# Performance work log

Measured on AMD Instinct MI355X. Metric: run time of the kernel, lower is better.

Reference implementation:

```python
import jax, jax.numpy as jnp
import numpy as np

R, B, F, C, NCLS = 32, 4096, 256, 4, 1000  # n_rules, batch, n_fea, n_channel, n_cls
K, PAD, POOL = 5, 1, 2                     # kernel_size, padding, pooling_size


def setup_inputs() -> dict:
    key = jax.random.key(0)
    ks = jax.random.split(key, 12)
    L0 = F + 2 * PAD - K + 1          # 254 after conv1
    L1 = L0 // POOL                   # 127 after avgpool1
    L2 = (L1 + 2 * PAD - K + 1) // POOL  # 62 after conv2+avgpool2
    att = C * L2                      # 248 (matches torch att_size formula)
    hid = att // 2                    # 124
    s = lambda k, shape: jax.random.normal(k, shape, dtype=jnp.float32) * 0.05
    return dict(
        data=jax.random.normal(ks[0], (B, F), dtype=jnp.float32),
        proto=s(ks[1], (R, F)),
        conv1_w=s(ks[2], (C, 1, K)), conv1_b=s(ks[3], (C,)),
        conv2_w=s(ks[4], (C, C, K)), conv2_b=s(ks[5], (C,)),
        fc1_w=s(ks[6], (att, hid)), fc1_b=s(ks[7], (hid,)),
        fc2_w=s(ks[8], (hid, 1)), fc2_b=s(ks[9], (1,)),
        consq_w=s(ks[10], (R, F, NCLS)), consq_b=s(ks[11], (R, NCLS)),
        is_train=0,
    )


def _conv1d(x, w, b):
    # x: [N, Cin, L], w: [Cout, Cin, K]
    out = jax.lax.conv_general_dilated(
        x, w, window_strides=(1,), padding=[(PAD, PAD)],
        dimension_numbers=('NCH', 'OIH', 'NCH'))
    return out + b[None, :, None]


def _avgpool2(x):
    # non-overlapping AvgPool1d(2), drops trailing remainder like torch
    L2 = x.shape[-1] // POOL
    return x[..., :L2 * POOL].reshape(x.shape[0], x.shape[1], L2, POOL).mean(-1)


def reference(data, proto, conv1_w, conv1_b, conv2_w, conv2_b,
              fc1_w, fc1_b, fc2_w, fc2_b, consq_w, consq_b, is_train):
    n_batch = data.shape[0]
    # data_diff: [R, B, F] -> shared gating net, fold rules into batch
    diff = (data[None, :, :] - proto[:, None, :]).reshape(R * n_batch, 1, F)
    h = _avgpool2(jax.nn.relu(_conv1d(diff, conv1_w, conv1_b)))
    h = _avgpool2(jax.nn.relu(_conv1d(h, conv2_w, conv2_b)))
    h = h.reshape(R * n_batch, -1)                       # [R*B, att]
    h = jax.nn.relu(h @ fc1_w + fc1_b)                   # [R*B, hid]
    fs_ini = jnp.tanh(h @ fc2_w + fc2_b)                 # [R*B, 1]
    fs_ini = fs_ini.reshape(R, n_batch).T                # cat(dim=1) -> [B, R]
    fs = jax.nn.softmax(fs_ini, axis=1)                  # softmax over rules
    # per-rule experts: grouped matmul [B,F] x [R,F,NCLS]
    expert = jnp.einsum('bf,rfc->rbc', data, consq_w) + consq_b[:, None, :]
    return jnp.einsum('br,rbc->bc', fs, expert)          # [B, NCLS]
```

## Files before the change

### kernel.cpp

```cpp
#include <hip/hip_runtime.h>
#include <hip/hip_bf16.h>

using bf16x8 = __attribute__((ext_vector_type(8))) short;
using f32x4  = __attribute__((ext_vector_type(4))) float;
using v2f    = __attribute__((ext_vector_type(2))) float;

__device__ __forceinline__ unsigned short f2bf_rne(float x) {
    unsigned u = __float_as_uint(x);
    u += 0x7fffu + ((u >> 16) & 1u);
    return (unsigned short)(u >> 16);
}

__device__ __forceinline__ void gload_lds16(const void* g, void* l) {
    __builtin_amdgcn_global_load_lds(
        (const __attribute__((address_space(1))) unsigned int*)g,
        (__attribute__((address_space(3))) unsigned int*)l, 16, 0, 0);
}

constexpr int KP = 8320;
constexpr int KROW = KP * 2;

constexpr size_t OFF_DT  = 0;
constexpr size_t OFF_Q1  = OFF_DT  + (size_t)260 * 4096 * 4;
constexpr size_t OFF_BT  = OFF_Q1  + (size_t)32 * 1024 * 4;
constexpr size_t OFF_C1P = OFF_BT;
constexpr size_t OFF_W1S = OFF_BT  + (size_t)1024 * KP * 2;
constexpr size_t OFF_FSI = OFF_W1S + (size_t)128 * 256 * 2;
constexpr size_t OFF_FS  = OFF_FSI + (size_t)32 * 4096 * 4;
constexpr size_t OFF_ASC = OFF_FS  + (size_t)32 * 4096 * 4;
constexpr size_t OFF_H2  = OFF_ASC;
constexpr size_t OFF_P1  = OFF_ASC + (size_t)4096 * KP * 2;

__global__ __launch_bounds__(256) void k_transpose(const float* __restrict__ data,
                                                   float* __restrict__ dTp) {
    __shared__ float tile[64][65];
    int bx = blockIdx.x & 63;
    int fx = blockIdx.x >> 6;
    int tx = threadIdx.x & 63, ty4 = threadIdx.x >> 6;
#pragma unroll
    for (int i = 0; i < 16; ++i) {
        int ty = ty4 * 16 + i;
        tile[ty][tx] = data[(bx * 64 + ty) * 256 + fx * 64 + tx];
    }
    __syncthreads();
#pragma unroll
    for (int i = 0; i < 16; ++i) {
        int ty = ty4 * 16 + i;
        dTp[(size_t)(fx * 64 + ty + 1) * 4096 + bx * 64 + tx] = tile[tx][ty];
    }
}

__global__ __launch_bounds__(256) void k_zrows(float* __restrict__ dTp) {
    int i = blockIdx.x * 256 + threadIdx.x;
    dTp[i] = 0.f;
    dTp[(size_t)257 * 4096 + i] = 0.f;
}

__global__ __launch_bounds__(256) void k_prep_proto(const float* __restrict__ proto,
                                                    const float* __restrict__ w1,
                                                    const float* __restrict__ b1,
                                                    float* __restrict__ q1p) {
    __shared__ float ps[256];
    __shared__ float w1s[20];
    int r = blockIdx.x, tid = threadIdx.x;
    ps[tid] = proto[r * 256 + tid];
    if (tid < 20) w1s[tid] = w1[tid];
    __syncthreads();
    if (tid < 254) {
#pragma unroll
        for (int c = 0; c < 4; ++c) {
            float s = -b1[c];
#pragma unroll
            for (int k = 0; k < 5; ++k) {
                int x = tid + k - 1;
                float xv = (x >= 0 && x < 256) ? ps[x] : 0.f;
                s += w1s[c * 5 + k] * xv;
            }
            q1p[r * 1024 + c * 256 + tid] = s;
        }
    }
}

__global__ __launch_bounds__(64) void k_prep_c1d(const float* __restrict__ dTp,
                                                 const float* __restrict__ w1,
                                                 float2* __restrict__ c1p) {
    int lane = threadIdx.x;
    int bg = blockIdx.x >> 3, ch = blockIdx.x & 7;
    int l0 = ch << 4;
    int nl = (ch == 7) ? 15 : 16;
    int b = (bg << 6) + lane;
    float w1r[20];
#pragma unroll
    for (int i = 0; i < 20; ++i) w1r[i] = w1[i];
    const float* dp = dTp + (size_t)(2 * l0) * 4096 + b;
    float d[6];
#pragma unroll
    for (int i = 0; i < 6; ++i) d[i] = dp[(size_t)i * 4096];
    dp += (size_t)6 * 4096;
    float2* outp = c1p + b;
    for (int li = 0; li < nl; ++li) {
        int l = l0 + li;
#pragma unroll
        for (int c = 0; c < 4; ++c) {
            float s0 = 0.f, s1 = 0.f;
#pragma unroll
            for (int k = 0; k < 5; ++k) {
                s0 += w1r[c * 5 + k] * d[k];
                s1 += w1r[c * 5 + k] * d[k + 1];
            }
            outp[(size_t)(c * 127 + l) * 4096] = make_float2(s0, s1);
        }
        d[0] = d[2]; d[1] = d[3]; d[2] = d[4]; d[3] = d[5];
        d[4] = dp[0];
        d[5] = dp[4096];
        dp += 8192;
    }
}

__global__ __launch_bounds__(256) void k_castB(const float* __restrict__ cw,
                                               const float* __restrict__ cb,
                                               unsigned short* __restrict__ BT) {
    __shared__ unsigned short L[64 * 137];
    int tid = threadIdx.x;
    int kt = blockIdx.x >> 3, ct = blockIdx.x & 7;
    int k0 = kt << 6, c0 = ct << 7;
#pragma unroll
    for (int i = 0; i < 32; ++i) {
        int flat = i * 256 + tid;
        int cl = flat & 127, kl = flat >> 7;
        int cg = c0 + cl;
        int kg = k0 + kl;
        float v = 0.f;
        if (cg < 1000) {
            if (kg < 8192) v = cw[(size_t)kg * 1000 + cg];
            else if (kg < 8224) v = cb[(size_t)(kg - 8192) * 1000 + cg];
        }
        L[kl * 137 + cl] = f2bf_rne(v);
    }
    __syncthreads();
#pragma unroll
    for (int i = 0; i < 4; ++i) {
        int task = i * 256 + tid;
        int kg = task & 7, cl = task >> 3;
        int base = kg * 8 * 137 + cl;
        unsigned x = (unsigned)L[base] | ((unsigned)L[base + 137] << 16);
        unsigned y = (unsigned)L[base + 2 * 137] | ((unsigned)L[base + 3 * 137] << 16);
        unsigned z = (unsigned)L[base + 4 * 137] | ((unsigned)L[base + 5 * 137] << 16);
        unsigned w = (unsigned)L[base + 6 * 137] | ((unsigned)L[base + 7 * 137] << 16);
        uint4 o; o.x = x; o.y = y; o.z = z; o.w = w;
        int cg = c0 + cl;
        size_t byte = (size_t)cg * KROW + (size_t)(kt << 7) + (size_t)((kg ^ (cg & 7)) << 4);
        *(uint4*)((char*)BT + byte) = o;
    }
}

__global__ __launch_bounds__(256) void k_castW(const float* __restrict__ fc1w,
                                               unsigned short* __restrict__ W1s) {
    int idx = blockIdx.x * 256 + threadIdx.x;
    int col = idx >> 8, k = idx & 255;
    float v = 0.f;
    if (col < 124 && k < 248) {
        int f = (k & 3) * 62 + (k >> 2);
        v = fc1w[f * 124 + col];
    }
    int byte = col * 512 + ((k >> 6) << 7) + ((((k >> 3) & 7) ^ (col & 7)) << 4) + ((k & 7) << 1);
    *(unsigned short*)((char*)W1s + byte) = f2bf_rne(v);
}

__global__ __launch_bounds__(64)
void k_conv2(const float2* __restrict__ c1p,
             const float* __restrict__ q1p,
             const float* __restrict__ w2,
             const float* __restrict__ b2,
             char* __restrict__ h2c) {
    __shared__ unsigned short T[64 * 72];

    int lane = threadIdx.x;
    int job = blockIdx.x;
    int jh = job & 1;
    int bc = (job >> 1) & 63;
    int r  = job >> 7;
    int b0 = bc << 6;
    int rb0 = r * 4096 + b0;
    int j2s = jh ? 32 : 0;

    float w2r[80];
#pragma unroll
    for (int i = 0; i < 80; ++i) w2r[i] = w2[i];
    v2f bb[4];
#pragma unroll
    for (int c = 0; c < 4; ++c) { float t = b2[c]; bb[c][0] = t; bb[c][1] = t; }

    const float* q1row = q1p + r * 1024;
    const float2* cpb = c1p + b0 + lane;

    auto pooled = [&](int c, int l) -> float {
        float2 v = cpb[(size_t)(c * 127 + l) * 4096];
        float2 q = *(const float2*)(q1row + c * 256 + 2 * l);
        return 0.5f * (fmaxf(v.x - q.x, 0.f) + fmaxf(v.y - q.y, 0.f));
    };

    v2f P[4][5];
#pragma unroll
    for (int c = 0; c < 4; ++c) {
        float pv[6];
#pragma unroll
        for (int idx = 0; idx < 6; ++idx) {
            int l = 2 * j2s - 1 + idx;
            pv[idx] = (l < 0) ? 0.f : pooled(c, l);
        }
#pragma unroll
        for (int k = 0; k < 5; ++k) { P[c][k][0] = pv[k]; P[c][k][1] = pv[k + 1]; }
    }

    int j2 = j2s;
#pragma unroll 1
    for (int chunk = 0; chunk < 2; ++chunk) {
        int cnt = (jh && chunk) ? 14 : 16;
#pragma unroll 1
        for (int jj = 0; jj < cnt; ++jj) {
            v2f u[4];
#pragma unroll
            for (int c = 0; c < 4; ++c) u[c] = bb[c];
#pragma unroll
            for (int c = 0; c < 4; ++c)
#pragma unroll
                for (int ci = 0; ci < 4; ++ci)
#pragma unroll
                    for (int k = 0; k < 5; ++k)
                        u[c] += P[ci][k] * w2r[(c * 4 + ci) * 5 + k];
            {
                float h0 = 0.5f * (fmaxf(u[0][0], 0.f) + fmaxf(u[0][1], 0.f));
                float h1 = 0.5f * (fmaxf(u[1][0], 0.f) + fmaxf(u[1][1], 0.f));
                float h2v = 0.5f * (fmaxf(u[2][0], 0.f) + fmaxf(u[2][1], 0.f));
                float h3 = 0.5f * (fmaxf(u[3][0], 0.f) + fmaxf(u[3][1], 0.f));
                uint2 vv;
                vv.x = (unsigned)f2bf_rne(h0) | ((unsigned)f2bf_rne(h1) << 16);
                vv.y = (unsigned)f2bf_rne(h2v) | ((unsigned)f2bf_rne(h3) << 16);
                *(uint2*)(T + lane * 72 + jj * 4) = vv;
            }
            if (!(chunk == 1 && jj == cnt - 1)) {
#pragma unroll
                for (int c = 0; c < 4; ++c) {
                    float n0 = pooled(c, 2 * j2 + 5);
                    float n1 = pooled(c, 2 * j2 + 6);
                    v2f p4v = P[c][4];
                    P[c][0] = P[c][2]; P[c][1] = P[c][3]; P[c][2] = p4v;
                    v2f t3; t3[0] = p4v[1]; t3[1] = n0;
                    v2f t4; t4[0] = n0;     t4[1] = n1;
                    P[c][3] = t3; P[c][4] = t4;
                }
            }
            ++j2;
        }
        if (jh && chunk) {
            uint4 z; z.x = z.y = z.z = z.w = 0u;
            *(uint4*)(T + lane * 72 + 56) = z;
        }
        {
            int chunkIdx = (j2s >> 4) + chunk;
            int g = lane & 7;
#pragma unroll
            for (int i = 0; i < 8; ++i) {
                int sL = i * 8 + (lane >> 3);
                bf16x8 v = *(const bf16x8*)(T + sL * 72 + g * 8);
                int srow = rb0 + sL;
                size_t byte = (size_t)srow * 512 + (size_t)(chunkIdx * 128)
                            + (size_t)((g ^ (srow & 7)) << 4);
                *(bf16x8*)(h2c + byte) = v;
            }
        }
    }
}

__global__ __launch_bounds__(256) void k_fc(const char* __restrict__ h2,
                                            const char* __restrict__ W1s,
                                            const float* __restrict__ fc1b,
                                            const float* __restrict__ fc2w,
                                            const float* __restrict__ fc2b,
                                            float* __restrict__ fsiniT) {
    int tid = threadIdx.x, lane = tid & 63, w = tid >> 6;
    int row0 = blockIdx.x * 128 + w * 32;
    int lr = lane & 15, g = lane >> 4, rxor = lr & 7;

    f32x4 acc[2][8] = {};

    const char* arow0 = h2 + (size_t)(row0 + lr) * 512;
    const char* arow1 = arow0 + 16 * 512;

    auto inrowf = [&](int ks) {
        return ((ks >> 1) << 7) + ((((ks * 4 + g) & 7) ^ rxor) << 4);
    };

    bf16x8 a0 = *(const bf16x8*)(arow0 + inrowf(0));
    bf16x8 a1 = *(const bf16x8*)(arow1 + inrowf(0));

#pragma unroll
    for (int ks = 0; ks < 8; ++ks) {
        int ir = inrowf(ks);
        bf16x8 bfr[8];
#pragma unroll
        for (int nf = 0; nf < 8; ++nf)
            bfr[nf] = *(const bf16x8*)(W1s + (nf * 16 + lr) * 512 + ir);
        bf16x8 an0 = a0, an1 = a1;
        if (ks < 7) {
            int ir2 = inrowf(ks + 1);
            an0 = *(const bf16x8*)(arow0 + ir2);
            an1 = *(const bf16x8*)(arow1 + ir2);
        }
#pragma unroll
        for (int nf = 0; nf < 8; ++nf) {
            acc[0][nf] = __builtin_amdgcn_mfma_f32_16x16x32_bf16(a0, bfr[nf], acc[0][nf], 0, 0, 0);
            acc[1][nf] = __builtin_amdgcn_mfma_f32_16x16x32_bf16(a1, bfr[nf], acc[1][nf], 0, 0, 0);
        }
        a0 = an0; a1 = an1;
    }

    float zp[2][4] = {};
#pragma unroll
    for (int nf = 0; nf < 8; ++nf) {
        int col = nf * 16 + lr;
        float b1v = (col < 124) ? fc1b[col] : 0.f;
        float w2v = (col < 124) ? fc2w[col] : 0.f;
#pragma unroll
        for (int mf = 0; mf < 2; ++mf)
#pragma unroll
            for (int q = 0; q < 4; ++q) {
                float h = fmaxf(acc[mf][nf][q] + b1v, 0.f);
                zp[mf][q] += h * w2v;
            }
    }
#pragma unroll
    for (int off = 1; off < 16; off <<= 1) {
#pragma unroll
        for (int mf = 0; mf < 2; ++mf)
#pragma unroll
            for (int q = 0; q < 4; ++q)
                zp[mf][q] += __shfl_xor(zp[mf][q], off, 64);
    }
    if (lr == 0) {
        float c2 = fc2b[0];
#pragma unroll
        for (int mf = 0; mf < 2; ++mf)
#pragma unroll
            for (int q = 0; q < 4; ++q) {
                int srow = row0 + mf * 16 + g * 4 + q;
                fsiniT[srow] = tanhf(zp[mf][q] + c2);
            }
    }
}

__global__ __launch_bounds__(256) void k_softmax(const float* __restrict__ fsiniT,
                                                 float* __restrict__ fsT) {
    int b = blockIdx.x * 256 + threadIdx.x;
    float v[32];
    float m = -1e30f;
#pragma unroll
    for (int r = 0; r < 32; ++r) { v[r] = fsiniT[r * 4096 + b]; m = fmaxf(m, v[r]); }
    float s = 0.f;
#pragma unroll
    for (int r = 0; r < 32; ++r) { v[r] = expf(v[r] - m); s += v[r]; }
    float inv = 1.f / s;
#pragma unroll
    for (int r = 0; r < 32; ++r) fsT[r * 4096 + b] = v[r] * inv;
}

__global__ __launch_bounds__(256) void k_scaleA(const float* __restrict__ data,
                                                const float* __restrict__ fsT,
                                                unsigned short* __restrict__ Asc) {
    int g = blockIdx.x * 256 + threadIdx.x;
    int b = g / 1040, kg = g - b * 1040;
    uint4 o;
    unsigned* op = (unsigned*)&o;
    if (kg < 1024) {
        int r = kg >> 5, f0 = (kg & 31) << 3;
        float fs = fsT[r * 4096 + b];
        const float4* dp = (const float4*)(data + b * 256 + f0);
        float4 v0 = dp[0], v1 = dp[1];
        float vals[8] = {v0.x, v0.y, v0.z, v0.w, v1.x, v1.y, v1.z, v1.w};
#pragma unroll
        for (int i = 0; i < 4; ++i) {
            unsigned lo = f2bf_rne(vals[2 * i] * fs);
            unsigned hi = f2bf_rne(vals[2 * i + 1] * fs);
            op[i] = lo | (hi << 16);
        }
    } else {
        int base = (kg - 1024) << 3;
        op[0] = op[1] = op[2] = op[3] = 0u;
        if (base < 32) {
#pragma unroll
            for (int i = 0; i < 4; ++i) {
                unsigned lo = f2bf_rne(fsT[(base + 2 * i) * 4096 + b]);
                unsigned hi = f2bf_rne(fsT[(base + 2 * i + 1) * 4096 + b]);
                op[i] = lo | (hi << 16);
            }
        }
    }
    size_t byte = (size_t)b * KROW + (size_t)((kg & ~7) << 4) + (size_t)(((kg & 7) ^ (b & 7)) << 4);
    *(uint4*)((char*)Asc + byte) = o;
}

__global__ __launch_bounds__(512) void k_gemm(const unsigned short* __restrict__ Asc,
                                              const unsigned short* __restrict__ BT,
                                              float* __restrict__ out,
                                              _Float16* __restrict__ part1) {
    __shared__ unsigned short As[2][8192];
    __shared__ unsigned short Bs[2][8192];
    int tid = threadIdx.x, lane = tid & 63, w = tid >> 6;
    int wm = w >> 2, wn = w & 3;
    int bid = blockIdx.x;
    int xcd = bid & 7, idx = bid >> 3;
    int mt = (xcd << 2) | (idx >> 4);
    int nt = (idx >> 1) & 7;
    int ks = idx & 1;
    int row0 = mt << 7, col0 = nt << 7;

    f32x4 acc[4][2] = {};

    const char* Ab = (const char*)Asc + (size_t)ks * (KP);
    const char* Bb = (const char*)BT + (size_t)ks * (KP);
    int flat0 = tid * 16, flat1 = tid * 16 + 8192;
    int rowl0 = flat0 >> 7, colB0 = flat0 & 127;
    int rowl1 = flat1 >> 7, colB1 = flat1 & 127;
    const char* aSrc0 = Ab + (size_t)(row0 + rowl0) * KROW + colB0;
    const char* aSrc1 = Ab + (size_t)(row0 + rowl1) * KROW + colB1;
    const char* bSrc0 = Bb + (size_t)(col0 + rowl0) * KROW + colB0;
    const char* bSrc1 = Bb + (size_t)(col0 + rowl1) * KROW + colB1;

    auto stage = [&](int buf, int kt) {
        int off = kt << 7;
        gload_lds16(aSrc0 + off, (char*)&As[buf][0] + flat0);
        gload_lds16(aSrc1 + off, (char*)&As[buf][0] + flat1);
        gload_lds16(bSrc0 + off, (char*)&Bs[buf][0] + flat0);
        gload_lds16(bSrc1 + off, (char*)&Bs[buf][0] + flat1);
    };

    auto compute = [&](int buf) {
        const char* Asb = (const char*)&As[buf][0];
        const char* Bsb = (const char*)&Bs[buf][0];
#pragma unroll
        for (int s = 0; s < 2; ++s) {
            bf16x8 af[4], bfv[2];
            int colByte = ((s << 5) + ((lane >> 4) << 3)) << 1;
#pragma unroll
            for (int mi = 0; mi < 4; ++mi) {
                int rowA = (wm << 6) + (mi << 4) + (lane & 15);
                int byte = (rowA << 7) + colByte;
                af[mi] = *(const bf16x8*)(Asb + (byte ^ ((rowA & 7) << 4)));
            }
#pragma unroll
            for (int ni = 0; ni < 2; ++ni) {
                int rowB = (wn << 5) + (ni << 4) + (lane & 15);
                int byte = (rowB << 7) + colByte;
                bfv[ni] = *(const bf16x8*)(Bsb + (byte ^ ((rowB & 7) << 4)));
            }
#pragma unroll
            for (int mi = 0; mi < 4; ++mi)
#pragma unroll
                for (int ni = 0; ni < 2; ++ni)
                    acc[mi][ni] = __builtin_amdgcn_mfma_f32_16x16x32_bf16(af[mi], bfv[ni], acc[mi][ni], 0, 0, 0);
        }
    };

    stage(0, 0);
    asm volatile("s_waitcnt vmcnt(0)" ::: "memory");
    __syncthreads();
#pragma unroll 1
    for (int kt = 0; kt < 64; ++kt) {
        stage((kt + 1) & 1, kt + 1);
        compute(kt & 1);
        asm volatile("s_waitcnt vmcnt(0)" ::: "memory");
        __syncthreads();
    }
    compute(0);

    int cA = col0 + (wn << 5) + (lane & 15);
    int cB2 = cA + 16;
    int rbase = row0 + (wm << 6) + ((lane >> 4) << 2);

    if (ks == 0) {
#pragma unroll
        for (int mi = 0; mi < 4; ++mi)
#pragma unroll
            for (int q = 0; q < 4; ++q) {
                int row = rbase + mi * 16 + q;
                if (cA < 1000) out[row * 1000 + cA] = acc[mi][0][q];
                if (cB2 < 1000) out[row * 1000 + cB2] = acc[mi][1][q];
            }
    } else {
#pragma unroll
        for (int mi = 0; mi < 4; ++mi)
#pragma unroll
            for (int q = 0; q < 4; ++q) {
                int row = rbase + mi * 16 + q;
                if (cA < 1000) part1[row * 1000 + cA] = (_Float16)acc[mi][0][q];
                if (cB2 < 1000) part1[row * 1000 + cB2] = (_Float16)acc[mi][1][q];
            }
    }
}

__global__ __launch_bounds__(256) void k_reduce(float* __restrict__ out,
                                                const _Float16* __restrict__ p1) {
    int i = (blockIdx.x * 256 + threadIdx.x) * 4;
    float4 o = *(float4*)(out + i);
    o.x += (float)p1[i];
    o.y += (float)p1[i + 1];
    o.z += (float)p1[i + 2];
    o.w += (float)p1[i + 3];
    *(float4*)(out + i) = o;
}

extern "C" void kernel_launch(void* const* d_in, const int* in_sizes, int n_in,
                              void* d_out, int out_size, void* d_ws, size_t ws_size,
                              hipStream_t stream) {
    const float* data  = (const float*)d_in[0];
    const float* proto = (const float*)d_in[1];
    const float* w1    = (const float*)d_in[2];
    const float* b1    = (const float*)d_in[3];
    const float* w2    = (const float*)d_in[4];
    const float* b2    = (const float*)d_in[5];
    const float* fc1w  = (const float*)d_in[6];
    const float* fc1b  = (const float*)d_in[7];
    const float* fc2w  = (const float*)d_in[8];
    const float* fc2b  = (const float*)d_in[9];
    const float* cw    = (const float*)d_in[10];
    const float* cbias = (const float*)d_in[11];
    float* out = (float*)d_out;
    char* ws = (char*)d_ws;

    float* dTp             = (float*)(ws + OFF_DT);
    float* q1p             = (float*)(ws + OFF_Q1);
    float2* c1p            = (float2*)(ws + OFF_C1P);
    unsigned short* BT     = (unsigned short*)(ws + OFF_BT);
    unsigned short* W1s    = (unsigned short*)(ws + OFF_W1S);
    float* fsiniT          = (float*)(ws + OFF_FSI);
    float* fsT             = (float*)(ws + OFF_FS);
    unsigned short* Asc    = (unsigned short*)(ws + OFF_ASC);
    char* h2c              = (char*)(ws + OFF_H2);
    _Float16* part1        = (_Float16*)(ws + OFF_P1);

    hipLaunchKernelGGL(k_transpose, dim3(256), dim3(256), 0, stream, data, dTp);
    hipLaunchKernelGGL(k_zrows, dim3(16), dim3(256), 0, stream, dTp);
    hipLaunchKernelGGL(k_prep_proto, dim3(32), dim3(256), 0, stream, proto, w1, b1, q1p);
    hipLaunchKernelGGL(k_prep_c1d, dim3(512), dim3(64), 0, stream, dTp, w1, c1p);
    hipLaunchKernelGGL(k_conv2, dim3(4096), dim3(64), 0, stream, c1p, q1p, w2, b2, h2c);
    hipLaunchKernelGGL(k_castB, dim3(1040), dim3(256), 0, stream, cw, cbias, BT);
    hipLaunchKernelGGL(k_castW, dim3(128), dim3(256), 0, stream, fc1w, W1s);
    hipLaunchKernelGGL(k_fc, dim3(1024), dim3(256), 0, stream,
                       h2c, (const char*)W1s, fc1b, fc2w, fc2b, fsiniT);
    hipLaunchKernelGGL(k_softmax, dim3(16), dim3(256), 0, stream, fsiniT, fsT);
    hipLaunchKernelGGL(k_scaleA, dim3(16640), dim3(256), 0, stream, data, fsT, Asc);
    hipLaunchKernelGGL(k_gemm, dim3(512), dim3(512), 0, stream, Asc, BT, out, part1);
    hipLaunchKernelGGL(k_reduce, dim3(4000), dim3(256), 0, stream, out, part1);
}
```

Measured before the change: 253.2 us.

## Fuse softmax-weighted A scaling into GEMM, dropping the scaleA kernel and buffer

```diff
diff --git a/kernel.cpp b/kernel.cpp
--- a/kernel.cpp
+++ b/kernel.cpp
@@ -27,9 +27,8 @@
 constexpr size_t OFF_W1S = OFF_BT  + (size_t)1024 * KP * 2;
 constexpr size_t OFF_FSI = OFF_W1S + (size_t)128 * 256 * 2;
 constexpr size_t OFF_FS  = OFF_FSI + (size_t)32 * 4096 * 4;
-constexpr size_t OFF_ASC = OFF_FS  + (size_t)32 * 4096 * 4;
-constexpr size_t OFF_H2  = OFF_ASC;
-constexpr size_t OFF_P1  = OFF_ASC + (size_t)4096 * KP * 2;
+constexpr size_t OFF_H2  = OFF_FS  + (size_t)32 * 4096 * 4;
+constexpr size_t OFF_P1  = OFF_H2  + (size_t)4096 * KP * 2;
 
 __global__ __launch_bounds__(256) void k_transpose(const float* __restrict__ data,
                                                    float* __restrict__ dTp) {
@@ -365,42 +364,8 @@
     for (int r = 0; r < 32; ++r) fsT[r * 4096 + b] = v[r] * inv;
 }
 
-__global__ __launch_bounds__(256) void k_scaleA(const float* __restrict__ data,
-                                                const float* __restrict__ fsT,
-                                                unsigned short* __restrict__ Asc) {
-    int g = blockIdx.x * 256 + threadIdx.x;
-    int b = g / 1040, kg = g - b * 1040;
-    uint4 o;
-    unsigned* op = (unsigned*)&o;
-    if (kg < 1024) {
-        int r = kg >> 5, f0 = (kg & 31) << 3;
-        float fs = fsT[r * 4096 + b];
-        const float4* dp = (const float4*)(data + b * 256 + f0);
-        float4 v0 = dp[0], v1 = dp[1];
-        float vals[8] = {v0.x, v0.y, v0.z, v0.w, v1.x, v1.y, v1.z, v1.w};
-#pragma unroll
-        for (int i = 0; i < 4; ++i) {
-            unsigned lo = f2bf_rne(vals[2 * i] * fs);
-            unsigned hi = f2bf_rne(vals[2 * i + 1] * fs);
-            op[i] = lo | (hi << 16);
-        }
-    } else {
-        int base = (kg - 1024) << 3;
-        op[0] = op[1] = op[2] = op[3] = 0u;
-        if (base < 32) {
-#pragma unroll
-            for (int i = 0; i < 4; ++i) {
-                unsigned lo = f2bf_rne(fsT[(base + 2 * i) * 4096 + b]);
-                unsigned hi = f2bf_rne(fsT[(base + 2 * i + 1) * 4096 + b]);
-                op[i] = lo | (hi << 16);
-            }
-        }
-    }
-    size_t byte = (size_t)b * KROW + (size_t)((kg & ~7) << 4) + (size_t)(((kg & 7) ^ (b & 7)) << 4);
-    *(uint4*)((char*)Asc + byte) = o;
-}
-
-__global__ __launch_bounds__(512) void k_gemm(const unsigned short* __restrict__ Asc,
+__global__ __launch_bounds__(512) void k_gemm(const float* __restrict__ data,
+                                              const float* __restrict__ fsT,
                                               const unsigned short* __restrict__ BT,
                                               float* __restrict__ out,
                                               _Float16* __restrict__ part1) {
@@ -414,25 +379,67 @@
     int nt = (idx >> 1) & 7;
     int ks = idx & 1;
     int row0 = mt << 7, col0 = nt << 7;
+    int ksbase = ks * 4160;
 
     f32x4 acc[4][2] = {};
 
-    const char* Ab = (const char*)Asc + (size_t)ks * (KP);
-    const char* Bb = (const char*)BT + (size_t)ks * (KP);
+    int arow = tid >> 2, aseg = tid & 3;
+    int rx = arow & 7;
+    const float* drow = data + (size_t)(row0 + arow) * 256;
+    char* aDst0[2], *aDst1[2];
+#pragma unroll
+    for (int bf = 0; bf < 2; ++bf) {
+        char* base = (char*)&As[bf][0] + (arow << 7);
+        aDst0[bf] = base + (((aseg * 2) ^ rx) << 4);
+        aDst1[bf] = base + (((aseg * 2 + 1) ^ rx) << 4);
+    }
+
+    const char* Bb = (const char*)BT + (size_t)ks * KP;
     int flat0 = tid * 16, flat1 = tid * 16 + 8192;
     int rowl0 = flat0 >> 7, colB0 = flat0 & 127;
     int rowl1 = flat1 >> 7, colB1 = flat1 & 127;
-    const char* aSrc0 = Ab + (size_t)(row0 + rowl0) * KROW + colB0;
-    const char* aSrc1 = Ab + (size_t)(row0 + rowl1) * KROW + colB1;
     const char* bSrc0 = Bb + (size_t)(col0 + rowl0) * KROW + colB0;
     const char* bSrc1 = Bb + (size_t)(col0 + rowl1) * KROW + colB1;
 
-    auto stage = [&](int buf, int kt) {
+    auto stageB = [&](int buf, int kt) {
         int off = kt << 7;
-        gload_lds16(aSrc0 + off, (char*)&As[buf][0] + flat0);
-        gload_lds16(aSrc1 + off, (char*)&As[buf][0] + flat1);
         gload_lds16(bSrc0 + off, (char*)&Bs[buf][0] + flat0);
         gload_lds16(bSrc1 + off, (char*)&Bs[buf][0] + flat1);
+    };
+
+    auto stageA_load = [&](int kt, f32x4 va[4], float& fsv) {
+        int k0 = ksbase + (kt << 6);
+        if (k0 < 8192) {
+            int rr = k0 >> 8, f0 = k0 & 255;
+            const float* dp = drow + f0 + aseg * 16;
+            va[0] = *(const f32x4*)(dp);
+            va[1] = *(const f32x4*)(dp + 4);
+            va[2] = *(const f32x4*)(dp + 8);
+            va[3] = *(const f32x4*)(dp + 12);
+            fsv = fsT[rr * 4096 + row0 + arow];
+        } else {
+            fsv = 1.f;
+#pragma unroll
+            for (int v4 = 0; v4 < 4; ++v4)
+#pragma unroll
+                for (int j = 0; j < 4; ++j) {
+                    int k = k0 + aseg * 16 + v4 * 4 + j;
+                    va[v4][j] = (k < 8224) ? fsT[(size_t)(k - 8192) * 4096 + row0 + arow] : 0.f;
+                }
+        }
+    };
+
+    auto stageA_write = [&](int buf, const f32x4 va[4], float fsv) {
+        unsigned gr[8];
+        const float* vv = (const float*)va;
+#pragma unroll
+        for (int j = 0; j < 8; ++j) {
+            unsigned lo = f2bf_rne(vv[2 * j] * fsv);
+            unsigned hi = f2bf_rne(vv[2 * j + 1] * fsv);
+            gr[j] = lo | (hi << 16);
+        }
+        *(uint4*)aDst0[buf] = *(uint4*)(gr);
+        *(uint4*)aDst1[buf] = *(uint4*)(gr + 4);
     };
 
     auto compute = [&](int buf) {
@@ -462,14 +469,21 @@
         }
     };
 
-    stage(0, 0);
-    asm volatile("s_waitcnt vmcnt(0)" ::: "memory");
+    {
+        f32x4 va[4]; float fsv;
+        stageA_load(0, va, fsv);
+        stageB(0, 0);
+        stageA_write(0, va, fsv);
+    }
     __syncthreads();
+
 #pragma unroll 1
     for (int kt = 0; kt < 64; ++kt) {
-        stage((kt + 1) & 1, kt + 1);
+        f32x4 va[4]; float fsv;
+        stageA_load(kt + 1, va, fsv);
+        stageB((kt + 1) & 1, kt + 1);
         compute(kt & 1);
-        asm volatile("s_waitcnt vmcnt(0)" ::: "memory");
+        stageA_write((kt + 1) & 1, va, fsv);
         __syncthreads();
     }
     compute(0);
@@ -535,7 +549,6 @@
     unsigned short* W1s    = (unsigned short*)(ws + OFF_W1S);
     float* fsiniT          = (float*)(ws + OFF_FSI);
     float* fsT             = (float*)(ws + OFF_FS);
-    unsigned short* Asc    = (unsigned short*)(ws + OFF_ASC);
     char* h2c              = (char*)(ws + OFF_H2);
     _Float16* part1        = (_Float16*)(ws + OFF_P1);
 
@@ -549,7 +562,6 @@
     hipLaunchKernelGGL(k_fc, dim3(1024), dim3(256), 0, stream,
                        h2c, (const char*)W1s, fc1b, fc2w, fc2b, fsiniT);
     hipLaunchKernelGGL(k_softmax, dim3(16), dim3(256), 0, stream, fsiniT, fsT);
-    hipLaunchKernelGGL(k_scaleA, dim3(16640), dim3(256), 0, stream, data, fsT, Asc);
-    hipLaunchKernelGGL(k_gemm, dim3(512), dim3(512), 0, stream, Asc, BT, out, part1);
+    hipLaunchKernelGGL(k_gemm, dim3(512), dim3(512), 0, stream, data, fsT, BT, out, part1);
     hipLaunchKernelGGL(k_reduce, dim3(4000), dim3(256), 0, stream, out, part1);
 }
```

Measured after the change: 271.4 us. 1.07x slower.

## Fuse conv2 and fc gating layers into one kernel via LDS staging

Applied to the files above, without the earlier changes.

```diff
diff --git a/kernel.cpp b/kernel.cpp
--- a/kernel.cpp
+++ b/kernel.cpp
@@ -28,7 +28,6 @@
 constexpr size_t OFF_FSI = OFF_W1S + (size_t)128 * 256 * 2;
 constexpr size_t OFF_FS  = OFF_FSI + (size_t)32 * 4096 * 4;
 constexpr size_t OFF_ASC = OFF_FS  + (size_t)32 * 4096 * 4;
-constexpr size_t OFF_H2  = OFF_ASC;
 constexpr size_t OFF_P1  = OFF_ASC + (size_t)4096 * KP * 2;
 
 __global__ __launch_bounds__(256) void k_transpose(const float* __restrict__ data,
@@ -167,56 +166,57 @@
     *(unsigned short*)((char*)W1s + byte) = f2bf_rne(v);
 }
 
-__global__ __launch_bounds__(64)
-void k_conv2(const float2* __restrict__ c1p,
-             const float* __restrict__ q1p,
-             const float* __restrict__ w2,
-             const float* __restrict__ b2,
-             char* __restrict__ h2c) {
-    __shared__ unsigned short T[64 * 72];
-
-    int lane = threadIdx.x;
-    int job = blockIdx.x;
-    int jh = job & 1;
-    int bc = (job >> 1) & 63;
-    int r  = job >> 7;
-    int b0 = bc << 6;
-    int rb0 = r * 4096 + b0;
+__global__ __launch_bounds__(128)
+void k_convfc(const float2* __restrict__ c1p,
+              const float* __restrict__ q1p,
+              const float* __restrict__ w2,
+              const float* __restrict__ b2,
+              const char* __restrict__ W1s,
+              const float* __restrict__ fc1b,
+              const float* __restrict__ fc2w,
+              const float* __restrict__ fc2b,
+              float* __restrict__ fsiniT) {
+    __shared__ unsigned short T[64 * 264];
+
+    int tid = threadIdx.x;
+    int w = tid >> 6, lane = tid & 63;
+    int r  = blockIdx.x >> 6;
+    int b0 = (blockIdx.x & 63) << 6;
+    int jh = w;
     int j2s = jh ? 32 : 0;
 
-    float w2r[80];
-#pragma unroll
-    for (int i = 0; i < 80; ++i) w2r[i] = w2[i];
-    v2f bb[4];
-#pragma unroll
-    for (int c = 0; c < 4; ++c) { float t = b2[c]; bb[c][0] = t; bb[c][1] = t; }
-
-    const float* q1row = q1p + r * 1024;
-    const float2* cpb = c1p + b0 + lane;
-
-    auto pooled = [&](int c, int l) -> float {
-        float2 v = cpb[(size_t)(c * 127 + l) * 4096];
-        float2 q = *(const float2*)(q1row + c * 256 + 2 * l);
-        return 0.5f * (fmaxf(v.x - q.x, 0.f) + fmaxf(v.y - q.y, 0.f));
-    };
-
-    v2f P[4][5];
-#pragma unroll
-    for (int c = 0; c < 4; ++c) {
-        float pv[6];
-#pragma unroll
-        for (int idx = 0; idx < 6; ++idx) {
-            int l = 2 * j2s - 1 + idx;
-            pv[idx] = (l < 0) ? 0.f : pooled(c, l);
-        }
-#pragma unroll
-        for (int k = 0; k < 5; ++k) { P[c][k][0] = pv[k]; P[c][k][1] = pv[k + 1]; }
-    }
-
-    int j2 = j2s;
-#pragma unroll 1
-    for (int chunk = 0; chunk < 2; ++chunk) {
-        int cnt = (jh && chunk) ? 14 : 16;
+    {
+        float w2r[80];
+#pragma unroll
+        for (int i = 0; i < 80; ++i) w2r[i] = w2[i];
+        v2f bb[4];
+#pragma unroll
+        for (int c = 0; c < 4; ++c) { float t = b2[c]; bb[c][0] = t; bb[c][1] = t; }
+
+        const float* q1row = q1p + r * 1024;
+        const float2* cpb = c1p + b0 + lane;
+
+        auto pooled = [&](int c, int l) -> float {
+            float2 v = cpb[(size_t)(c * 127 + l) * 4096];
+            float2 q = *(const float2*)(q1row + c * 256 + 2 * l);
+            return 0.5f * (fmaxf(v.x - q.x, 0.f) + fmaxf(v.y - q.y, 0.f));
+        };
+
+        v2f P[4][5];
+#pragma unroll
+        for (int c = 0; c < 4; ++c) {
+            float pv[6];
+#pragma unroll
+            for (int idx = 0; idx < 6; ++idx) {
+                int l = 2 * j2s - 1 + idx;
+                pv[idx] = (l < 0) ? 0.f : pooled(c, l);
+            }
+#pragma unroll
+            for (int k = 0; k < 5; ++k) { P[c][k][0] = pv[k]; P[c][k][1] = pv[k + 1]; }
+        }
+
+        int cnt = jh ? 30 : 32;
+        int j2 = j2s;
 #pragma unroll 1
         for (int jj = 0; jj < cnt; ++jj) {
             v2f u[4];
@@ -237,9 +237,9 @@
                 uint2 vv;
                 vv.x = (unsigned)f2bf_rne(h0) | ((unsigned)f2bf_rne(h1) << 16);
                 vv.y = (unsigned)f2bf_rne(h2v) | ((unsigned)f2bf_rne(h3) << 16);
-                *(uint2*)(T + lane * 72 + jj * 4) = vv;
-            }
-            if (!(chunk == 1 && jj == cnt - 1)) {
+                *(uint2*)(T + lane * 264 + j2 * 4) = vv;
+            }
+            if (jj < cnt - 1) {
 #pragma unroll
                 for (int c = 0; c < 4; ++c) {
                     float n0 = pooled(c, 2 * j2 + 5);
@@ -253,100 +253,76 @@
             }
             ++j2;
         }
-        if (jh && chunk) {
+        if (jh) {
             uint4 z; z.x = z.y = z.z = z.w = 0u;
-            *(uint4*)(T + lane * 72 + 56) = z;
-        }
-        {
-            int chunkIdx = (j2s >> 4) + chunk;
-            int g = lane & 7;
-#pragma unroll
-            for (int i = 0; i < 8; ++i) {
-                int sL = i * 8 + (lane >> 3);
-                bf16x8 v = *(const bf16x8*)(T + sL * 72 + g * 8);
-                int srow = rb0 + sL;
-                size_t byte = (size_t)srow * 512 + (size_t)(chunkIdx * 128)
-                            + (size_t)((g ^ (srow & 7)) << 4);
-                *(bf16x8*)(h2c + byte) = v;
-            }
-        }
-    }
-}
-
-__global__ __launch_bounds__(256) void k_fc(const char* __restrict__ h2,
-                                            const char* __restrict__ W1s,
-                                            const float* __restrict__ fc1b,
-                                            const float* __restrict__ fc2w,
-                                            const float* __restrict__ fc2b,
-                                            float* __restrict__ fsiniT) {
-    int tid = threadIdx.x, lane = tid & 63, w = tid >> 6;
-    int row0 = blockIdx.x * 128 + w * 32;
-    int lr = lane & 15, g = lane >> 4, rxor = lr & 7;
-
-    f32x4 acc[2][8] = {};
-
-    const char* arow0 = h2 + (size_t)(row0 + lr) * 512;
-    const char* arow1 = arow0 + 16 * 512;
-
-    auto inrowf = [&](int ks) {
-        return ((ks >> 1) << 7) + ((((ks * 4 + g) & 7) ^ rxor) << 4);
-    };
-
-    bf16x8 a0 = *(const bf16x8*)(arow0 + inrowf(0));
-    bf16x8 a1 = *(const bf16x8*)(arow1 + inrowf(0));
-
-#pragma unroll
-    for (int ks = 0; ks < 8; ++ks) {
-        int ir = inrowf(ks);
-        bf16x8 bfr[8];
-#pragma unroll
-        for (int nf = 0; nf < 8; ++nf)
-            bfr[nf] = *(const bf16x8*)(W1s + (nf * 16 + lr) * 512 + ir);
-        bf16x8 an0 = a0, an1 = a1;
-        if (ks < 7) {
-            int ir2 = inrowf(ks + 1);
-            an0 = *(const bf16x8*)(arow0 + ir2);
-            an1 = *(const bf16x8*)(arow1 + ir2);
-        }
+            *(uint4*)(T + lane * 264 + 248) = z;
+        }
+    }
+    __syncthreads();
+
+    {
+        int row0 = w << 5;
+        int lr = lane & 15, g = lane >> 4, rxor = lr & 7;
+
+        f32x4 acc[2][8] = {};
+
+        const unsigned short* trow0 = T + (row0 + lr) * 264;
+        const unsigned short* trow1 = trow0 + 16 * 264;
+
+        auto inrowf = [&](int ks) {
+            return ((ks >> 1) << 7) + ((((ks * 4 + g) & 7) ^ rxor) << 4);
+        };
+
+#pragma unroll
+        for (int ks = 0; ks < 8; ++ks) {
+            int koff = ks * 32 + g * 8;
+            bf16x8 a0 = *(const bf16x8*)(trow0 + koff);
+            bf16x8 a1 = *(const bf16x8*)(trow1 + koff);
+            int ir = inrowf(ks);
+            bf16x8 bfr[8];
+#pragma unroll
+            for (int nf = 0; nf < 8; ++nf)
+                bfr[nf] = *(const bf16x8*)(W1s + (nf * 16 + lr) * 512 + ir);
+#pragma unroll
+            for (int nf = 0; nf < 8; ++nf) {
+                acc[0][nf] = __builtin_amdgcn_mfma_f32_16x16x32_bf16(a0, bfr[nf], acc[0][nf], 0, 0, 0);
+                acc[1][nf] = __builtin_amdgcn_mfma_f32_16x16x32_bf16(a1, bfr[nf], acc[1][nf], 0, 0, 0);
+            }
+        }
+
+        float zp[2][4] = {};
 #pragma unroll
         for (int nf = 0; nf < 8; ++nf) {
-            acc[0][nf] = __builtin_amdgcn_mfma_f32_16x16x32_bf16(a0, bfr[nf], acc[0][nf], 0, 0, 0);
-            acc[1][nf] = __builtin_amdgcn_mfma_f32_16x16x32_bf16(a1, bfr[nf], acc[1][nf], 0, 0, 0);
-        }
-        a0 = an0; a1 = an1;
-    }
-
-    float zp[2][4] = {};
-#pragma unroll
-    for (int nf = 0; nf < 8; ++nf) {
-        int col = nf * 16 + lr;
-        float b1v = (col < 124) ? fc1b[col] : 0.f;
-        float w2v = (col < 124) ? fc2w[col] : 0.f;
-#pragma unroll
-        for (int mf = 0; mf < 2; ++mf)
-#pragma unroll
-            for (int q = 0; q < 4; ++q) {
-                float h = fmaxf(acc[mf][nf][q] + b1v, 0.f);
-                zp[mf][q] += h * w2v;
-            }
-    }
-#pragma unroll
-    for (int off = 1; off < 16; off <<= 1) {
-#pragma unroll
-        for (int mf = 0; mf < 2; ++mf)
-#pragma unroll
-            for (int q = 0; q < 4; ++q)
-                zp[mf][q] += __shfl_xor(zp[mf][q], off, 64);
-    }
-    if (lr == 0) {
-        float c2 = fc2b[0];
-#pragma unroll
-        for (int mf = 0; mf < 2; ++mf)
-#pragma unroll
-            for (int q = 0; q < 4; ++q) {
-                int srow = row0 + mf * 16 + g * 4 + q;
-                fsiniT[srow] = tanhf(zp[mf][q] + c2);
-            }
+            int col = nf * 16 + lr;
+            float b1v = (col < 124) ? fc1b[col] : 0.f;
+            float w2v = (col < 124) ? fc2w[col] : 0.f;
+#pragma unroll
+            for (int mf = 0; mf < 2; ++mf)
+#pragma unroll
+                for (int q = 0; q < 4; ++q) {
+                    float h = fmaxf(acc[mf][nf][q] + b1v, 0.f);
+                    zp[mf][q] += h * w2v;
+                }
+        }
+#pragma unroll
+        for (int off = 1; off < 16; off <<= 1) {
+#pragma unroll
+            for (int mf = 0; mf < 2; ++mf)
+#pragma unroll
+                for (int q = 0; q < 4; ++q)
+                    zp[mf][q] += __shfl_xor(zp[mf][q], off, 64);
+        }
+        if (lr == 0) {
+            float c2 = fc2b[0];
+            int sbase = r * 4096 + b0 + row0;
+#pragma unroll
+            for (int mf = 0; mf < 2; ++mf)
+#pragma unroll
+                for (int q = 0; q < 4; ++q) {
+                    int srow = sbase + mf * 16 + g * 4 + q;
+                    fsiniT[srow] = tanhf(zp[mf][q] + c2);
+                }
+        }
     }
 }
 
@@ -536,18 +512,16 @@
     float* fsiniT          = (float*)(ws + OFF_FSI);
     float* fsT             = (float*)(ws + OFF_FS);
     unsigned short* Asc    = (unsigned short*)(ws + OFF_ASC);
-    char* h2c              = (char*)(ws + OFF_H2);
     _Float16* part1        = (_Float16*)(ws + OFF_P1);
 
     hipLaunchKernelGGL(k_transpose, dim3(256), dim3(256), 0, stream, data, dTp);
     hipLaunchKernelGGL(k_zrows, dim3(16), dim3(256), 0, stream, dTp);
     hipLaunchKernelGGL(k_prep_proto, dim3(32), dim3(256), 0, stream, proto, w1, b1, q1p);
     hipLaunchKernelGGL(k_prep_c1d, dim3(512), dim3(64), 0, stream, dTp, w1, c1p);
-    hipLaunchKernelGGL(k_conv2, dim3(4096), dim3(64), 0, stream, c1p, q1p, w2, b2, h2c);
+    hipLaunchKernelGGL(k_castW, dim3(128), dim3(256), 0, stream, fc1w, W1s);
+    hipLaunchKernelGGL(k_convfc, dim3(2048), dim3(128), 0, stream,
+                       c1p, q1p, w2, b2, (const char*)W1s, fc1b, fc2w, fc2b, fsiniT);
     hipLaunchKernelGGL(k_castB, dim3(1040), dim3(256), 0, stream, cw, cbias, BT);
-    hipLaunchKernelGGL(k_castW, dim3(128), dim3(256), 0, stream, fc1w, W1s);
-    hipLaunchKernelGGL(k_fc, dim3(1024), dim3(256), 0, stream,
-                       h2c, (const char*)W1s, fc1b, fc2w, fc2b, fsiniT);
     hipLaunchKernelGGL(k_softmax, dim3(16), dim3(256), 0, stream, fsiniT, fsT);
     hipLaunchKernelGGL(k_scaleA, dim3(16640), dim3(256), 0, stream, data, fsT, Asc);
     hipLaunchKernelGGL(k_gemm, dim3(512), dim3(512), 0, stream, Asc, BT, out, part1);
```

Result: no change. 256.9 us (+1.4%).
